# Optimization experiments

Measured on AMD Instinct MI355X. Metric: run time of the kernel, lower is better.

The kernel has to match this reference:

```python
import jax, jax.numpy as jnp
import numpy as np

N_HEADS = 16
HEAD_DIM = 64
WINDOW = 128
GLOBAL = 64


def setup_inputs() -> dict:
    key = jax.random.key(0)
    ks = jax.random.split(key, 5)
    B, T, D = 2, 8192, 1024
    s = 0.02
    return {
        "x": jax.random.normal(ks[0], (B, T, D), dtype=jnp.float32),
        "Wq": jax.random.normal(ks[1], (D, D), dtype=jnp.float32) * s,
        "Wk": jax.random.normal(ks[2], (D, D), dtype=jnp.float32) * s,
        "Wv": jax.random.normal(ks[3], (D, D), dtype=jnp.float32) * s,
        "Wo": jax.random.normal(ks[4], (D, D), dtype=jnp.float32) * s,
    }


def reference(x, Wq, Wk, Wv, Wo):
    B, T, D = x.shape
    h, hd, w = N_HEADS, HEAD_DIM, WINDOW
    g = min(GLOBAL, T)
    nw = T // w  # T chosen as a multiple of window_size
    scale = hd ** -0.5

    def proj(W):
        # nn.Linear: y = x @ W.T ; then (B,T,h,hd) -> (B,h,T,hd)
        return (x @ W.T).reshape(B, T, h, hd).transpose(0, 2, 1, 3)

    q = proj(Wq)
    k = proj(Wk)
    v = proj(Wv)

    # Chunk into non-overlapping local windows: (B,h,nw,w,hd)
    qw = q.reshape(B, h, nw, w, hd)
    kw = k.reshape(B, h, nw, w, hd)
    vw = v.reshape(B, h, nw, w, hd)
    kg = k[:, :, :g, :]  # global prefix keys (B,h,g,hd)
    vg = v[:, :, :g, :]

    # Scores against [global ++ local] keys (faithful: global prefix is
    # concatenated for every window, including windows that overlap it).
    s_g = jnp.einsum("bhnqd,bhgd->bhnqg", qw, kg) * scale  # (B,h,nw,w,g)
    s_l = jnp.einsum("bhnqd,bhnkd->bhnqk", qw, kw) * scale  # (B,h,nw,w,w)
    attn = jax.nn.softmax(jnp.concatenate([s_g, s_l], axis=-1), axis=-1)

    out = (
        jnp.einsum("bhnqg,bhgd->bhnqd", attn[..., :g], vg)
        + jnp.einsum("bhnqk,bhnkd->bhnqd", attn[..., g:], vw)
    )
    out = out.reshape(B, h, T, hd).transpose(0, 2, 1, 3).reshape(B, T, D)
    return out @ Wo.T
```

## Files before the change

kernel.cpp:

```cpp
#include <hip/hip_runtime.h>

typedef unsigned short u16;
typedef __attribute__((ext_vector_type(8))) short short8;
typedef __attribute__((ext_vector_type(4))) float f32x4;
typedef __attribute__((ext_vector_type(4))) float floatx4;
typedef __attribute__((ext_vector_type(4))) unsigned short ushort4v;
typedef __attribute__((ext_vector_type(8))) unsigned short ushort8v;

#define MFMA(a, b, c) __builtin_amdgcn_mfma_f32_16x16x32_bf16(a, b, c, 0, 0, 0)

__device__ __forceinline__ u16 f2bf(float f) {
    unsigned u = __float_as_uint(f);
    u += 0x7fffu + ((u >> 16) & 1u);
    return (u16)(u >> 16);
}

__device__ __forceinline__ void async16(const void* g, void* l) {
    __builtin_amdgcn_global_load_lds(
        (const __attribute__((address_space(1))) void*)g,
        (__attribute__((address_space(3))) void*)l, 16, 0, 0);
}

__global__ void cvt_bf16(const float* __restrict__ s, u16* __restrict__ d, int n4) {
    int i = blockIdx.x * blockDim.x + threadIdx.x;
    int stride = gridDim.x * blockDim.x;
    for (; i < n4; i += stride) {
        floatx4 v = ((const floatx4*)s)[i];
        ushort4v o;
        o[0] = f2bf(v[0]); o[1] = f2bf(v[1]); o[2] = f2bf(v[2]); o[3] = f2bf(v[3]);
        ((ushort4v*)d)[i] = o;
    }
}

__global__ void cvt4_bf16(const float* __restrict__ s0, const float* __restrict__ s1,
                          const float* __restrict__ s2, const float* __restrict__ s3,
                          u16* __restrict__ d, int n4) {
    const float* s = blockIdx.y == 0 ? s0 : (blockIdx.y == 1 ? s1 : (blockIdx.y == 2 ? s2 : s3));
    u16* dd = d + (size_t)blockIdx.y * n4 * 4;
    int i = blockIdx.x * blockDim.x + threadIdx.x;
    int stride = gridDim.x * blockDim.x;
    for (; i < n4; i += stride) {
        floatx4 v = ((const floatx4*)s)[i];
        ushort4v o;
        o[0] = f2bf(v[0]); o[1] = f2bf(v[1]); o[2] = f2bf(v[2]); o[3] = f2bf(v[3]);
        ((ushort4v*)dd)[i] = o;
    }
}

template <bool BF16_OUT>
__global__ __launch_bounds__(256) void gemm_nt(
    const u16* __restrict__ A, const u16* __restrict__ B0,
    const u16* __restrict__ B1, const u16* __restrict__ B2,
    void* __restrict__ Cv, int M, int N, int K)
{
    __shared__ u16 As[128 * 32];
    __shared__ u16 Bs[128 * 32];
    const int tid = threadIdx.x;
    const int wave = tid >> 6, lane = tid & 63;
    const int quad = lane >> 4, tl = lane & 15;
    const int m0 = blockIdx.x * 128, n0 = blockIdx.y * 128;
    const int wm = wave >> 1, wn = wave & 1;
    const u16* Bm = blockIdx.z == 0 ? B0 : (blockIdx.z == 1 ? B1 : B2);
    const size_t coff = (size_t)blockIdx.z * M * N;

    f32x4 acc[4][4];
#pragma unroll
    for (int i = 0; i < 4; i++)
#pragma unroll
        for (int j = 0; j < 4; j++) acc[i][j] = (f32x4)(0.0f);

    const int rslot = quad ^ ((tl >> 1) & 3);

    for (int k0 = 0; k0 < K; k0 += 32) {
#pragma unroll
        for (int i = 0; i < 2; i++) {
            int cb = (i * 4 + wave) * 64;
            int ch = cb + lane;
            int row = ch >> 2, slot = ch & 3;
            int g = slot ^ ((row >> 1) & 3);
            async16(A  + (size_t)(m0 + row) * K + k0 + g * 8, (u16*)As + cb * 8);
            async16(Bm + (size_t)(n0 + row) * K + k0 + g * 8, (u16*)Bs + cb * 8);
        }
        __syncthreads();
        short8 af[4], bg[4];
#pragma unroll
        for (int t = 0; t < 4; t++) {
            af[t] = *(const short8*)&As[(wm * 64 + t * 16 + tl) * 32 + rslot * 8];
            bg[t] = *(const short8*)&Bs[(wn * 64 + t * 16 + tl) * 32 + rslot * 8];
        }
#pragma unroll
        for (int mt = 0; mt < 4; mt++)
#pragma unroll
            for (int nt = 0; nt < 4; nt++)
                acc[mt][nt] = MFMA(af[mt], bg[nt], acc[mt][nt]);
        __syncthreads();
    }

#pragma unroll
    for (int mt = 0; mt < 4; mt++)
#pragma unroll
        for (int nt = 0; nt < 4; nt++)
#pragma unroll
            for (int r = 0; r < 4; r++) {
                int row = m0 + wm * 64 + mt * 16 + quad * 4 + r;
                int col = n0 + wn * 64 + nt * 16 + tl;
                if constexpr (BF16_OUT)
                    ((u16*)Cv)[coff + (size_t)row * N + col] = f2bf(acc[mt][nt][r]);
                else
                    ((float*)Cv)[coff + (size_t)row * N + col] = acc[mt][nt][r];
            }
}

__global__ __launch_bounds__(256) void attn_win(
    const u16* __restrict__ qkv, u16* __restrict__ outb)
{
    constexpr int T = 8192, D = 1024, HD = 64, G = 64, WIN = 128;
    constexpr int MTOT = 2 * T;
    __shared__ u16 Vt[64 * 200];
    __shared__ u16 KP[12800];

    const int blk = blockIdx.x;
    const int half = blk & 1;
    const int nwin = (blk >> 1) & 63;
    const int h = (blk >> 7) & 15;
    const int b = blk >> 11;
    const int tid = threadIdx.x;
    const int wave = tid >> 6, lane = tid & 63;
    const int quad = lane >> 4, tl = lane & 15;
    const int win0 = nwin * WIN;
    const int q0 = win0 + half * 64;
    const size_t brow = (size_t)b * T;
    const u16* qb = qkv;
    const u16* kb = qkv + (size_t)MTOT * D;
    const u16* vb = qkv + (size_t)2 * MTOT * D;

#pragma unroll
    for (int i = 0; i < 6; i++) {
        int ch = i * 256 + tid;
        int row = ch >> 3, slot = ch & 7;
        int g = slot ^ (row & 7);
        int tok = row < G ? row : win0 + (row - G);
        async16(kb + (brow + tok) * D + h * HD + g * 8,
                (u16*)KP + (i * 256 + wave * 64) * 8);
    }

    for (int i = 0; i < 6; i++) {
        int ch = i * 256 + tid;
        int r = ch >> 3, c = ch & 7;
        int tok = r < G ? r : win0 + (r - G);
        ushort8v v = *(const ushort8v*)(vb + (brow + tok) * D + h * HD + c * 8);
#pragma unroll
        for (int j = 0; j < 8; j++) Vt[(c * 8 + j) * 200 + r] = v[j];
    }

    short8 bq[2];
    {
        int tok = q0 + wave * 16 + tl;
        const u16* qrow = qb + (brow + tok) * D + h * HD;
        bq[0] = *(const short8*)(qrow + quad * 8);
        bq[1] = *(const short8*)(qrow + 32 + quad * 8);
    }

    __syncthreads();

    f32x4 s[12];
#pragma unroll
    for (int kt = 0; kt < 12; kt++) s[kt] = (f32x4)(0.0f);
#pragma unroll
    for (int kt = 0; kt < 12; kt++) {
        int row = kt * 16 + tl;
        int s0 = quad ^ (tl & 7);
        int s1 = (4 + quad) ^ (tl & 7);
        short8 a0 = *(const short8*)&KP[row * 64 + s0 * 8];
        short8 a1 = *(const short8*)&KP[row * 64 + s1 * 8];
        s[kt] = MFMA(a0, bq[0], s[kt]);
        s[kt] = MFMA(a1, bq[1], s[kt]);
    }

    const float c1 = 0.125f * 1.4426950408889634f;
    float mx = -1e30f;
#pragma unroll
    for (int kt = 0; kt < 12; kt++)
#pragma unroll
        for (int r = 0; r < 4; r++) mx = fmaxf(mx, s[kt][r]);
    mx = fmaxf(mx, __shfl_xor(mx, 16, 64));
    mx = fmaxf(mx, __shfl_xor(mx, 32, 64));
    float sum = 0.f;
#pragma unroll
    for (int kt = 0; kt < 12; kt++)
#pragma unroll
        for (int r = 0; r < 4; r++) {
            float e = exp2f((s[kt][r] - mx) * c1);
            s[kt][r] = e;
            sum += e;
        }
    sum += __shfl_xor(sum, 16, 64);
    sum += __shfl_xor(sum, 32, 64);
    float inv = 1.f / sum;

    __syncthreads();

    u16* Pl = (u16*)KP;
    {
        int lq = wave * 16 + tl;
#pragma unroll
        for (int kt = 0; kt < 12; kt++) {
            ushort4v p;
#pragma unroll
            for (int r = 0; r < 4; r++) p[r] = f2bf(s[kt][r] * inv);
            *(ushort4v*)&Pl[lq * 200 + kt * 16 + quad * 4] = p;
        }
    }
    __syncthreads();

    f32x4 o[4];
#pragma unroll
    for (int dt = 0; dt < 4; dt++) o[dt] = (f32x4)(0.0f);
#pragma unroll
    for (int ks = 0; ks < 6; ks++) {
        short8 pa = *(const short8*)&Pl[(wave * 16 + tl) * 200 + ks * 32 + quad * 8];
#pragma unroll
        for (int dt = 0; dt < 4; dt++) {
            short8 vv = *(const short8*)&Vt[(dt * 16 + tl) * 200 + ks * 32 + quad * 8];
            o[dt] = MFMA(pa, vv, o[dt]);
        }
    }

#pragma unroll
    for (int dt = 0; dt < 4; dt++)
#pragma unroll
        for (int r = 0; r < 4; r++) {
            int qq = q0 + wave * 16 + quad * 4 + r;
            int dim = dt * 16 + tl;
            outb[(brow + qq) * D + h * HD + dim] = f2bf(o[dt][r]);
        }
}

extern "C" void kernel_launch(void* const* d_in, const int* in_sizes, int n_in,
                              void* d_out, int out_size, void* d_ws, size_t ws_size,
                              hipStream_t stream)
{
    const float* x  = (const float*)d_in[0];
    const float* Wq = (const float*)d_in[1];
    const float* Wk = (const float*)d_in[2];
    const float* Wv = (const float*)d_in[3];
    const float* Wo = (const float*)d_in[4];

    const int M = 16384, D = 1024;
    u16* xb  = (u16*)d_ws;
    u16* wqb = xb  + (size_t)M * D;
    u16* wob = wqb + (size_t)3 * D * D;
    u16* qkv = wob + (size_t)D * D;
    u16* att = qkv + (size_t)3 * M * D;

    cvt_bf16<<<2048, 256, 0, stream>>>(x, xb, M * D / 4);
    cvt4_bf16<<<dim3(64, 4), 256, 0, stream>>>(Wq, Wk, Wv, Wo, wqb, D * D / 4);

    gemm_nt<true ><<<dim3(M / 128, D / 128, 3), 256, 0, stream>>>(
        xb, wqb, wqb + (size_t)D * D, wqb + (size_t)2 * D * D, qkv, M, D, D);
    attn_win<<<dim3(4096), 256, 0, stream>>>(qkv, att);
    gemm_nt<false><<<dim3(M / 128, D / 128, 1), 256, 0, stream>>>(
        att, wob, wob, wob, d_out, M, D, D);
}
```

Before: 377.5 us.

## Double GEMM K-tile to 64 and stage V transpose through LDS via async loads

The projection GEMM now loads a 64-wide K slice per iteration with an 8-slot XOR swizzle, which halves the number of barrier pairs per output tile. In the attention kernel, V is first async-loaded into the K/P shared buffer, then transposed inside shared memory into Vt with vectorized 16-byte stores, and K is reloaded afterwards. This replaces per-element scattered 2-byte LDS writes fed by synchronous global loads. The cost is two extra barriers and a serialized V-then-K load sequence, plus double the GEMM shared memory, which may lower occupancy.

Result: faster. 339.4 us (-10.1%).

```diff
diff --git a/kernel.cpp b/kernel.cpp
--- a/kernel.cpp
+++ b/kernel.cpp
@@ -53,8 +53,8 @@
     const u16* __restrict__ B1, const u16* __restrict__ B2,
     void* __restrict__ Cv, int M, int N, int K)
 {
-    __shared__ u16 As[128 * 32];
-    __shared__ u16 Bs[128 * 32];
+    __shared__ u16 As[128 * 64];
+    __shared__ u16 Bs[128 * 64];
     const int tid = threadIdx.x;
     const int wave = tid >> 6, lane = tid & 63;
     const int quad = lane >> 4, tl = lane & 15;
@@ -69,30 +69,33 @@
 #pragma unroll
         for (int j = 0; j < 4; j++) acc[i][j] = (f32x4)(0.0f);
 
-    const int rslot = quad ^ ((tl >> 1) & 3);
-
-    for (int k0 = 0; k0 < K; k0 += 32) {
-#pragma unroll
-        for (int i = 0; i < 2; i++) {
-            int cb = (i * 4 + wave) * 64;
-            int ch = cb + lane;
-            int row = ch >> 2, slot = ch & 3;
-            int g = slot ^ ((row >> 1) & 3);
-            async16(A  + (size_t)(m0 + row) * K + k0 + g * 8, (u16*)As + cb * 8);
-            async16(Bm + (size_t)(n0 + row) * K + k0 + g * 8, (u16*)Bs + cb * 8);
+    const int srow = tid >> 3, sslot = tid & 7;
+
+    for (int k0 = 0; k0 < K; k0 += 64) {
+#pragma unroll
+        for (int i = 0; i < 4; i++) {
+            int row = i * 32 + srow;
+            int g = sslot ^ (row & 7);
+            int ldsbase = (i * 256 + wave * 64) * 8;
+            async16(A  + (size_t)(m0 + row) * K + k0 + g * 8, (u16*)As + ldsbase);
+            async16(Bm + (size_t)(n0 + row) * K + k0 + g * 8, (u16*)Bs + ldsbase);
         }
         __syncthreads();
-        short8 af[4], bg[4];
-#pragma unroll
-        for (int t = 0; t < 4; t++) {
-            af[t] = *(const short8*)&As[(wm * 64 + t * 16 + tl) * 32 + rslot * 8];
-            bg[t] = *(const short8*)&Bs[(wn * 64 + t * 16 + tl) * 32 + rslot * 8];
-        }
-#pragma unroll
-        for (int mt = 0; mt < 4; mt++)
-#pragma unroll
-            for (int nt = 0; nt < 4; nt++)
-                acc[mt][nt] = MFMA(af[mt], bg[nt], acc[mt][nt]);
+#pragma unroll
+        for (int h = 0; h < 2; h++) {
+            short8 af[4], bg[4];
+            const int rs = (((h * 4 + quad) ^ (tl & 7)) * 8);
+#pragma unroll
+            for (int t = 0; t < 4; t++) {
+                af[t] = *(const short8*)&As[(wm * 64 + t * 16 + tl) * 64 + rs];
+                bg[t] = *(const short8*)&Bs[(wn * 64 + t * 16 + tl) * 64 + rs];
+            }
+#pragma unroll
+            for (int mt = 0; mt < 4; mt++)
+#pragma unroll
+                for (int nt = 0; nt < 4; nt++)
+                    acc[mt][nt] = MFMA(af[mt], bg[nt], acc[mt][nt]);
+        }
         __syncthreads();
     }
 
@@ -137,20 +140,10 @@
 #pragma unroll
     for (int i = 0; i < 6; i++) {
         int ch = i * 256 + tid;
-        int row = ch >> 3, slot = ch & 7;
-        int g = slot ^ (row & 7);
+        int row = ch >> 3, c = ch & 7;
         int tok = row < G ? row : win0 + (row - G);
-        async16(kb + (brow + tok) * D + h * HD + g * 8,
+        async16(vb + (brow + tok) * D + h * HD + c * 8,
                 (u16*)KP + (i * 256 + wave * 64) * 8);
-    }
-
-    for (int i = 0; i < 6; i++) {
-        int ch = i * 256 + tid;
-        int r = ch >> 3, c = ch & 7;
-        int tok = r < G ? r : win0 + (r - G);
-        ushort8v v = *(const ushort8v*)(vb + (brow + tok) * D + h * HD + c * 8);
-#pragma unroll
-        for (int j = 0; j < 8; j++) Vt[(c * 8 + j) * 200 + r] = v[j];
     }
 
     short8 bq[2];
@@ -159,6 +152,32 @@
         const u16* qrow = qb + (brow + tok) * D + h * HD;
         bq[0] = *(const short8*)(qrow + quad * 8);
         bq[1] = *(const short8*)(qrow + 32 + quad * 8);
+    }
+
+    __syncthreads();
+
+    {
+        const int d = tid & 63;
+#pragma unroll
+        for (int i = 0; i < 6; i++) {
+            int c = i * 4 + wave;
+            ushort8v v;
+#pragma unroll
+            for (int j = 0; j < 8; j++) v[j] = KP[(c * 8 + j) * 64 + d];
+            *(ushort8v*)&Vt[d * 200 + c * 8] = v;
+        }
+    }
+
+    __syncthreads();
+
+#pragma unroll
+    for (int i = 0; i < 6; i++) {
+        int ch = i * 256 + tid;
+        int row = ch >> 3, slot = ch & 7;
+        int g = slot ^ (row & 7);
+        int tok = row < G ? row : win0 + (row - G);
+        async16(kb + (brow + tok) * D + h * HD + g * 8,
+                (u16*)KP + (i * 256 + wave * 64) * 8);
     }
 
     __syncthreads();
```
